# Performance work log

Hardware: AMD Instinct MI355X
Metric: run time of the kernel (lower is better)

## Reference

```python
import jax, jax.numpy as jnp
import numpy as np

B, C_HID, H, W = 2, 30, 1024, 1024
PS, PAD = 16, 4            # patch_size, patch_padding
MID, OUT = 80, 1
POST = 8                   # post_conv_layers
H_ERR, W_ERR = H // PS, W // PS
K_PER_B = int(H_ERR * W_ERR * 0.125)   # sampling top-k per batch = 512
P = B * K_PER_B
C_IN = C_HID + 1           # conv0 input channels = 31
KWIN = PS + 2 * PAD        # 24 = patch window incl. padding
N_PRE = PAD - 1            # conv1..conv3 (conv0 separate)
EPS = 1e-5


def _bn_params(key, c):
    k1, k2, k3, k4 = jax.random.split(key, 4)
    g = 1.0 + 0.1 * jax.random.normal(k1, (c,), jnp.float32)
    b = 0.1 * jax.random.normal(k2, (c,), jnp.float32)
    m = 0.1 * jax.random.normal(k3, (c,), jnp.float32)
    v = jax.random.uniform(k4, (c,), jnp.float32, 0.5, 1.5)
    return jnp.stack([g, b, m, v])  # (4, c)


def setup_inputs() -> dict:
    key = jax.random.key(0)
    ks = jax.random.split(key, 12)
    cw = lambda k, co, ci: 0.05 * jax.random.normal(k, (co, ci, 3, 3), jnp.float32)
    return {
        "pha": jax.random.normal(ks[0], (B, 1, H, W), jnp.float32),
        "err": jax.random.uniform(ks[1], (B, 1, H_ERR, W_ERR), jnp.float32),
        "hid": jax.random.normal(ks[2], (B, C_HID, H, W), jnp.float32),
        "w0": cw(ks[3], MID, C_IN),
        "bn0": _bn_params(ks[4], MID),
        "w_pre": 0.05 * jax.random.normal(ks[5], (N_PRE, MID, MID, 3, 3), jnp.float32),
        "bn_pre": jnp.stack([_bn_params(k, MID) for k in jax.random.split(ks[6], N_PRE)]),
        "w_post": 0.05 * jax.random.normal(ks[7], (POST - 1, MID, MID, 3, 3), jnp.float32),
        "bn_post": jnp.stack([_bn_params(k, MID) for k in jax.random.split(ks[8], POST - 1)]),
        "w_last": cw(ks[9], OUT, MID),
    }


def _conv(x, w, padding):
    return jax.lax.conv_general_dilated(x, w, (1, 1), padding,
        dimension_numbers=("NCHW", "OIHW", "NCHW"))


def _bn(x, p):  # eval-mode BatchNorm, p = (4, C)
    g, b, m, v = p
    inv = g * jax.lax.rsqrt(v + EPS)
    return x * inv[None, :, None, None] + (b - m * inv)[None, :, None, None]


def reference(pha, err, hid, w0, bn0, w_pre, bn_pre, w_post, bn_post, w_last):
    # --- select_refinement_regions (mode='sampling') ---
    err_flat = err.reshape(B, -1)                                   # (B, H_ERR*W_ERR)
    _, top_idx = jax.lax.top_k(err_flat, K_PER_B)                   # (B, K)
    ref = jnp.zeros_like(err_flat).at[jnp.arange(B)[:, None], top_idx].set(1.0)
    ref = ref * (err_flat > 0).astype(ref.dtype)                    # prevent_oversampling
    ref = ref.reshape(B, 1, H_ERR, W_ERR)
    # static-size nonzero: err>0 a.s. so exactly K per batch are selected
    b_idx = jnp.repeat(jnp.arange(B), K_PER_B)                      # (P,)
    flat = top_idx.reshape(-1)
    i_idx = flat // W_ERR
    j_idx = flat % W_ERR
    # --- crop_patch (unfold) on detached cat([hid, pha]) ---
    x = jax.lax.stop_gradient(jnp.concatenate([hid, pha], axis=1))  # (B, 31, H, W)
    xp = jnp.pad(x, ((0, 0), (0, 0), (PAD, PAD), (PAD, PAD)))
    rows = i_idx[:, None] * PS + jnp.arange(KWIN)[None, :]          # (P, 24)
    cols = j_idx[:, None] * PS + jnp.arange(KWIN)[None, :]
    patches = xp[b_idx[:, None, None], :, rows[:, :, None], cols[:, None, :]]  # (P,24,24,31)
    y = patches.transpose(0, 3, 1, 2)                               # (P, 31, 24, 24)
    # --- pre convs: valid 3x3, each shrinks by 2 (24 -> 16) ---
    y = jax.nn.relu(_bn(_conv(y, w0, "VALID"), bn0))
    for l in range(N_PRE):
        y = jax.nn.relu(_bn(_conv(y, w_pre[l], "VALID"), bn_pre[l]))
    # --- post convs: residual same-padded, last maps to out_channel ---
    for l in range(POST - 1):
        y = y + jax.nn.relu(_bn(_conv(y, w_post[l], "SAME"), bn_post[l]))
    y = _conv(y, w_last, "SAME")                                    # (P, 1, 16, 16)
    # --- replace_patch (scatter_nd) ---
    pha6 = pha.reshape(B, 1, H_ERR, PS, W_ERR, PS).transpose(0, 2, 4, 1, 3, 5)
    pha6 = pha6.at[b_idx, i_idx, j_idx].set(y)
    pha_out = pha6.transpose(0, 3, 1, 4, 2, 5).reshape(B, 1, H, W)
    return pha_out, ref
```

## Files before the change

kernel.cpp:

```cpp
#include <hip/hip_runtime.h>
#include <hip/hip_bf16.h>
#include <stdint.h>

typedef __hip_bfloat16 bf16;
typedef __attribute__((ext_vector_type(8))) short short8;
typedef __attribute__((ext_vector_type(4))) float f32x4;

__device__ __forceinline__ bf16 f2b(float x) { return __float2bfloat16(x); }

#define NW 8

#define A0_OFF 0
#define X_OFF  77440
#define A1_OFF 77440
#define A2_OFF 0
#define Z_OFF  57024
#define BB_OFF 114048
#define BS_OFF 147840
#define YF_OFF 0
#define SMEM_SZ 158080

__device__ __forceinline__ void gload_lds16(const void* g, char* l) {
    __builtin_amdgcn_global_load_lds(
        (const __attribute__((address_space(1))) unsigned int*)g,
        (__attribute__((address_space(3))) unsigned int*)l, 16, 0, 0);
}

__global__ __launch_bounds__(1024) void topk_kernel(const float* __restrict__ err,
                                                    float* __restrict__ ref_out,
                                                    int* __restrict__ sel)
{
    __shared__ uint64_t keys[4096];
    const int b = blockIdx.x >> 4, slice = blockIdx.x & 15;
    const float* e = err + b * 4096;
    for (int t = threadIdx.x; t < 4096; t += 1024) {
        uint32_t u = __float_as_uint(e[t]);
        u ^= (u >> 31) ? 0xFFFFFFFFu : 0x80000000u;
        keys[t] = ((uint64_t)u << 32) | (uint32_t)(4095 - t);
    }
    __syncthreads();
    const int cand = slice * 256 + (threadIdx.x >> 2);
    const int part = threadIdx.x & 3;
    const uint64_t mykey = keys[cand];
    int r = 0;
#pragma unroll 8
    for (int j = part * 1024; j < part * 1024 + 1024; ++j)
        r += (keys[j] > mykey) ? 1 : 0;
    r += __shfl_xor(r, 1);
    r += __shfl_xor(r, 2);
    if (part == 0) {
        bool s = (r < 512);
        if (s) sel[b * 512 + r] = cand;
        ref_out[b * 4096 + cand] = (s && e[cand] > 0.f) ? 1.f : 0.f;
    }
}

__global__ void wt_kernel(const float* __restrict__ w0, const float* __restrict__ wpre,
                          const float* __restrict__ wpost, const float* __restrict__ w_last,
                          const float* __restrict__ bn0, const float* __restrict__ bn_pre,
                          const float* __restrict__ bn_post,
                          bf16* __restrict__ Wf, float* __restrict__ wlastT,
                          float* __restrict__ bnprep)
{
    int t = blockIdx.x * blockDim.x + threadIdx.x;
    if (t < 714240) {
        int l, tap, kb, rem;
        if (t < 23040) { l = 0; tap = t / 2560; kb = 0; rem = t % 2560; }
        else {
            int t2 = t - 23040;
            l = 1 + t2 / 69120;
            int r0 = t2 % 69120;
            tap = r0 / 7680;
            int r1 = r0 % 7680;
            kb = r1 / 2560; rem = r1 % 2560;
        }
        int n = rem / 512, r2 = rem % 512, lane = r2 / 8, i = r2 % 8;
        int co = n * 16 + (lane & 15);
        int k  = kb * 32 + (lane >> 4) * 8 + i;
        float v = 0.f;
        if (l == 0)      { if (k < 31) v = w0[(co * 31 + k) * 9 + tap]; }
        else if (l <= 3) { if (k < 80) v = wpre[(((l - 1) * 80 + co) * 80 + k) * 9 + tap]; }
        else             { if (k < 80) v = wpost[(((l - 4) * 80 + co) * 80 + k) * 9 + tap]; }
        Wf[t] = f2b(v);
    } else if (t < 714960) {
        int i = t - 714240; int tap = i / 80, ci = i % 80;
        wlastT[tap * 80 + ci] = w_last[ci * 9 + tap];
    } else if (t < 715840) {
        int i = t - 714960; int l = i / 80, co = i % 80;
        const float* src = (l == 0) ? bn0 : (l <= 3 ? bn_pre + (l - 1) * 320
                                                    : bn_post + (l - 4) * 320);
        float g = src[co], bb = src[80 + co], m = src[160 + co], vv = src[240 + co];
        float inv = g * rsqrtf(vv + 1e-5f);
        bnprep[i * 2]     = inv;
        bnprep[i * 2 + 1] = bb - m * inv;
    }
}

__global__ void copy_kernel(const uint4* __restrict__ src, uint4* __restrict__ dst, int n)
{
    int t = blockIdx.x * blockDim.x + threadIdx.x;
    if (t < n) dst[t] = src[t];
}

template <int NIN, int NOUT, int KB, int PMAX, int MODE, int ISTR, int OSTR,
          int BIG, int STOREZ>
__device__ __forceinline__ void conv_mfma(char* sm, int inBase, int outBase,
                                          const char* __restrict__ Wl,
                                          const float* __restrict__ bnl,
                                          f32x4 (&Yreg)[2][5])
{
    const int tid = threadIdx.x;
    const int wv = tid >> 6, lane = tid & 63;
    const int r = lane & 15, kg = lane >> 4;
    constexpr int NPIX  = NOUT * NOUT;
    constexpr int NMT   = (NPIX + 15) / 16;
    constexpr int NSTEP = BIG ? 9 : 9 * KB;
    constexpr int SLOT  = BIG ? 16384 : 5120;
    constexpr int BOFF  = BIG ? BB_OFF : BS_OFF;
    constexpr int WSTEP = BIG ? 15360 : 5120;

    int aA[PMAX][2];
    bool act[PMAX][2];
#pragma unroll
    for (int pp = 0; pp < PMAX; ++pp)
#pragma unroll
        for (int mm = 0; mm < 2; ++mm) {
            int mt = (wv + pp * NW) * 2 + mm;
            int pix = mt * 16 + r;
            act[pp][mm] = (mt < NMT);
            int cp = pix < NPIX ? pix : NPIX - 1;
            aA[pp][mm] = inBase + ((cp / NOUT) * NIN + cp % NOUT) * ISTR + kg * 16;
        }
    const int vB = BOFF + lane * 16;

    float invb[5], betb[5];
#pragma unroll
    for (int n = 0; n < 5; ++n) {
        float2 v = ((const float2*)bnl)[n * 16 + r];
        invb[n] = v.x; betb[n] = v.y;
    }

    f32x4 zz = {0.f, 0.f, 0.f, 0.f};
    f32x4 acc[PMAX][2][5];
#pragma unroll
    for (int pp = 0; pp < PMAX; ++pp)
#pragma unroll
        for (int mm = 0; mm < 2; ++mm)
#pragma unroll
            for (int n = 0; n < 5; ++n) acc[pp][mm][n] = zz;

    auto stage = [&](int step, int slot) {
        const char* src = Wl + step * WSTEP;
        char* dst = sm + BOFF + slot * SLOT;
        if (BIG) {
            gload_lds16(src + tid * 16, dst + tid * 16);
            gload_lds16(src + 8192 + tid * 16, dst + 8192 + tid * 16);
        } else if (tid < 320) {
            gload_lds16(src + tid * 16, dst + tid * 16);
        }
    };

    auto inner = [&](int dtap, int kb, int slotBase) {
        short8 bf[5];
#pragma unroll
        for (int n = 0; n < 5; ++n)
            bf[n] = *(const short8*)(sm + slotBase + n * 1024 + lane * 16);
#pragma unroll
        for (int pp = 0; pp < PMAX; ++pp)
#pragma unroll
            for (int mm = 0; mm < 2; ++mm) {
                if (!act[pp][mm]) continue;
                short8 af = *(const short8*)(sm + aA[pp][mm] + dtap * ISTR + kb * 64);
#pragma unroll
                for (int n = 0; n < 5; ++n)
                    acc[pp][mm][n] = __builtin_amdgcn_mfma_f32_16x16x32_bf16(
                        af, bf[n], acc[pp][mm][n], 0, 0, 0);
            }
    };

    stage(0, 0);
    __syncthreads();

#pragma unroll
    for (int s = 0; s < NSTEP; ++s) {
        if (s + 1 < NSTEP) stage(s + 1, (s + 1) & 1);
        const int tap = BIG ? s : s / KB;
        const int dtap = (tap / 3) * NIN + (tap % 3);
        const int sb = BOFF + (s & 1) * SLOT;
        if (BIG) {
#pragma unroll
            for (int kb = 0; kb < 3; ++kb) inner(dtap, kb, sb + kb * 5120);
        } else {
            inner(dtap, s % KB, sb);
        }
        __syncthreads();
    }

#pragma unroll
    for (int pp = 0; pp < PMAX; ++pp)
#pragma unroll
        for (int mm = 0; mm < 2; ++mm) {
            int mt = (wv + pp * NW) * 2 + mm;
            if (mt < NMT) {
#pragma unroll
                for (int n = 0; n < 5; ++n) {
                    int co = n * 16 + r;
#pragma unroll
                    for (int j = 0; j < 4; ++j) {
                        int pix = mt * 16 + kg * 4 + j;
                        if (pix < NPIX) {
                            float o = fmaxf(acc[pp][mm][n][j] * invb[n] + betb[n], 0.f);
                            if (MODE == 0) {
                                *(bf16*)(sm + outBase + pix * OSTR + co * 2) = f2b(o);
                            } else if (MODE == 1) {
                                Yreg[mm][n][j] = o;
                                int rowb = ((pix >> 4) + 1) * (18 * 176) + ((pix & 15) + 1) * 176;
                                *(bf16*)(sm + outBase + rowb + co * 2) = f2b(o);
                            } else {
                                float nv = Yreg[mm][n][j] + o;
                                Yreg[mm][n][j] = nv;
                                if (STOREZ) {
                                    int rowb = ((pix >> 4) + 1) * (18 * 176) + ((pix & 15) + 1) * 176;
                                    *(bf16*)(sm + outBase + rowb + co * 2) = f2b(nv);
                                }
                            }
                        }
                    }
                }
            }
        }
}

__global__ __launch_bounds__(512, 2) void refine_kernel(
    const int* __restrict__ sel,
    const float* __restrict__ hid, const float* __restrict__ pha,
    const char* __restrict__ Wf, const float* __restrict__ wlastT,
    const float* __restrict__ bnprep, float* __restrict__ out)
{
    __shared__ __align__(16) char sm[SMEM_SZ];
    const int tid = threadIdx.x;
    const int p = blockIdx.x;
    const int e = sel[p];
    const int b = p >> 9;
    const int pi = e >> 6, pj = e & 63;

    {
        uint4 z4 = {0u, 0u, 0u, 0u};
        uint4* z = (uint4*)sm;
        for (int t = tid; t < SMEM_SZ / 16; t += 512) z[t] = z4;
    }
    __syncthreads();

    const int r0 = pi * 16 - 4, c0 = pj * 16 - 4;
    for (int t = tid; t < 32 * 576; t += 512) {
        int c = t / 576, pix = t - c * 576;
        int gr = r0 + pix / 24, gc = c0 + pix % 24;
        float v = 0.f;
        if (c < 31 && (unsigned)gr < 1024u && (unsigned)gc < 1024u)
            v = (c < 30) ? hid[((b * 30 + c) * 1024 + gr) * 1024 + gc]
                         : pha[(b * 1024 + gr) * 1024 + gc];
        *(bf16*)(sm + X_OFF + pix * 80 + c * 2) = f2b(v);
    }

    f32x4 Yreg[2][5];

    conv_mfma<24,22,1,2,0, 80,160,0,1>(sm, X_OFF,  A0_OFF, Wf,                    bnprep,       Yreg);
    conv_mfma<22,20,3,2,0,160,176,0,1>(sm, A0_OFF, A1_OFF, Wf + 46080,            bnprep + 160, Yreg);
    conv_mfma<20,18,3,2,0,176,176,0,1>(sm, A1_OFF, A2_OFF, Wf + 46080 + 138240,   bnprep + 320, Yreg);
    conv_mfma<18,16,3,1,1,176,176,1,1>(sm, A2_OFF, Z_OFF,  Wf + 46080 + 2*138240, bnprep + 480, Yreg);

    for (int t = tid; t < 68 * 44; t += 512) {
        int idx = t / 44, w = t - idx * 44;
        int row;
        if (idx < 18) row = idx;
        else if (idx < 36) row = 306 + (idx - 18);
        else { int k = idx - 36; row = (1 + (k >> 1)) * 18 + ((k & 1) ? 17 : 0); }
        *(uint32_t*)(sm + Z_OFF + row * 176 + w * 4) = 0u;
    }

#pragma unroll 1
    for (int l = 0; l < 6; ++l)
        conv_mfma<18,16,3,1,2,176,176,1,1>(sm, Z_OFF, Z_OFF,
                                           Wf + 46080 + (3 + l) * 138240,
                                           bnprep + 640 + l * 160, Yreg);
    conv_mfma<18,16,3,1,2,176,176,1,0>(sm, Z_OFF, Z_OFF,
                                       Wf + 46080 + 9 * 138240, bnprep + 1600, Yreg);

    {
        const int wv = tid >> 6, lane = tid & 63;
        const int r = lane & 15, kg = lane >> 4;
#pragma unroll
        for (int mm = 0; mm < 2; ++mm) {
            int mt = 2 * wv + mm;
#pragma unroll
            for (int n = 0; n < 5; ++n) {
                int co = n * 16 + r;
#pragma unroll
                for (int j = 0; j < 4; ++j) {
                    int pix = mt * 16 + kg * 4 + j;
                    *(float*)(sm + YF_OFF + pix * 336 + co * 4) = Yreg[mm][n][j];
                }
            }
        }
    }
    __syncthreads();

    {
        int pix = tid >> 1, half = tid & 1;
        int y = pix >> 4, x = pix & 15;
        float accv = 0.f;
        const float* Yb = (const float*)(sm + YF_OFF);
#pragma unroll
        for (int tap = 0; tap < 9; ++tap) {
            int iy = y + tap / 3 - 1, ix = x + tap % 3 - 1;
            if ((unsigned)iy >= 16u || (unsigned)ix >= 16u) continue;
            const float* yp = Yb + (iy * 16 + ix) * 84;
            const float* wp = wlastT + tap * 80;
            for (int c = half * 40; c < half * 40 + 40; c += 4) {
                float4 a  = *(const float4*)(yp + c);
                float4 w4 = *(const float4*)(wp + c);
                accv += a.x * w4.x + a.y * w4.y + a.z * w4.z + a.w * w4.w;
            }
        }
        accv += __shfl_xor(accv, 1);
        if (half == 0)
            out[b * 1048576 + (pi * 16 + y) * 1024 + pj * 16 + x] = accv;
    }
}

extern "C" void kernel_launch(void* const* d_in, const int* in_sizes, int n_in,
                              void* d_out, int out_size, void* d_ws, size_t ws_size,
                              hipStream_t stream)
{
    (void)in_sizes; (void)n_in; (void)out_size; (void)ws_size;
    const float* pha     = (const float*)d_in[0];
    const float* err     = (const float*)d_in[1];
    const float* hid     = (const float*)d_in[2];
    const float* w0      = (const float*)d_in[3];
    const float* bn0     = (const float*)d_in[4];
    const float* w_pre   = (const float*)d_in[5];
    const float* bn_pre  = (const float*)d_in[6];
    const float* w_post  = (const float*)d_in[7];
    const float* bn_post = (const float*)d_in[8];
    const float* w_last  = (const float*)d_in[9];
    float* out = (float*)d_out;

    char* ws = (char*)d_ws;
    bf16*  Wf     = (bf16*)ws;
    float* wlastT = (float*)(ws + 1429504);
    float* bnprep = (float*)(ws + 1432384);
    int*   sel    = (int*)(ws + 1441792);

    hipLaunchKernelGGL(wt_kernel, dim3(2797), dim3(256), 0, stream,
                       w0, w_pre, w_post, w_last, bn0, bn_pre, bn_post,
                       Wf, wlastT, bnprep);
    hipLaunchKernelGGL(topk_kernel, dim3(32), dim3(1024), 0, stream,
                       err, out + 2097152, sel);
    hipLaunchKernelGGL(copy_kernel, dim3(2048), dim3(256), 0, stream,
                       (const uint4*)pha, (uint4*)out, 524288);
    hipLaunchKernelGGL(refine_kernel, dim3(1024), dim3(512), 0, stream,
                       sel, hid, pha, (const char*)Wf, wlastT, bnprep, out);
}
```

Baseline: 510.5 us.

## Retile 16x16 post convs as 2D wave grid with DPP-shifted A-fragment reuse

Replaces the generic conv template for the last pre conv and the residual post convs with specialised kernels. These use a 4x2 wave grid (4 row tiles by 3 output-channel tiles, with channels padded to 96). In the post layers each wave loads 6 rows of A fragments once per K block and builds the dx-shifted operands with DPP lane shifts instead of re-reading LDS. Weights are relaid out per kb/tap in larger staged chunks. This cuts LDS reads per MFMA but adds padded-channel MFMAs (96 vs 80) and more barriers per layer.

```diff
diff --git a/kernel.cpp b/kernel.cpp
--- a/kernel.cpp
+++ b/kernel.cpp
@@ -11,19 +11,37 @@
 #define NW 8
 
 #define A0_OFF 0
-#define X_OFF  77440
-#define A1_OFF 77440
+#define X_OFF  81312
+#define A1_OFF 81312
 #define A2_OFF 0
 #define Z_OFF  57024
-#define BB_OFF 114048
-#define BS_OFF 147840
+#define B3_OFF 114048
+#define BS_OFF 151712
+#define BP_OFF 0
 #define YF_OFF 0
-#define SMEM_SZ 158080
+#define SMEM_SZ 161952
 
 __device__ __forceinline__ void gload_lds16(const void* g, char* l) {
     __builtin_amdgcn_global_load_lds(
         (const __attribute__((address_space(1))) unsigned int*)g,
         (__attribute__((address_space(3))) unsigned int*)l, 16, 0, 0);
+}
+
+__device__ __forceinline__ short8 dpp_sr1(short8 v) {
+    union { short8 s; int i[4]; } a, o;
+    a.s = v;
+#pragma unroll
+    for (int q = 0; q < 4; ++q)
+        o.i[q] = __builtin_amdgcn_mov_dpp(a.i[q], 0x111, 0xf, 0xf, true);
+    return o.s;
+}
+__device__ __forceinline__ short8 dpp_sl1(short8 v) {
+    union { short8 s; int i[4]; } a, o;
+    a.s = v;
+#pragma unroll
+    for (int q = 0; q < 4; ++q)
+        o.i[q] = __builtin_amdgcn_mov_dpp(a.i[q], 0x101, 0xf, 0xf, true);
+    return o.s;
 }
 
 __global__ __launch_bounds__(1024) void topk_kernel(const float* __restrict__ err,
@@ -63,36 +81,54 @@
                           float* __restrict__ bnprep)
 {
     int t = blockIdx.x * blockDim.x + threadIdx.x;
-    if (t < 714240) {
-        int l, tap, kb, rem;
-        if (t < 23040) { l = 0; tap = t / 2560; kb = 0; rem = t % 2560; }
-        else {
+    if (t < 824832) {
+        int co, k, tap;
+        float v = 0.f;
+        if (t < 23040) {
+            tap = t / 2560; int rem = t % 2560;
+            int n = rem / 512, r2 = rem % 512, lane = r2 / 8, i = r2 % 8;
+            co = n * 16 + (lane & 15); k = (lane >> 4) * 8 + i;
+            if (k < 31) v = w0[(co * 31 + k) * 9 + tap];
+        } else if (t < 161280) {
             int t2 = t - 23040;
-            l = 1 + t2 / 69120;
+            int l = t2 / 69120;
             int r0 = t2 % 69120;
-            tap = r0 / 7680;
-            int r1 = r0 % 7680;
-            kb = r1 / 2560; rem = r1 % 2560;
-        }
-        int n = rem / 512, r2 = rem % 512, lane = r2 / 8, i = r2 % 8;
-        int co = n * 16 + (lane & 15);
-        int k  = kb * 32 + (lane >> 4) * 8 + i;
-        float v = 0.f;
-        if (l == 0)      { if (k < 31) v = w0[(co * 31 + k) * 9 + tap]; }
-        else if (l <= 3) { if (k < 80) v = wpre[(((l - 1) * 80 + co) * 80 + k) * 9 + tap]; }
-        else             { if (k < 80) v = wpost[(((l - 4) * 80 + co) * 80 + k) * 9 + tap]; }
+            tap = r0 / 7680; int r1 = r0 % 7680;
+            int kb = r1 / 2560, rem = r1 % 2560;
+            int n = rem / 512, r2 = rem % 512, lane = r2 / 8, i = r2 % 8;
+            co = n * 16 + (lane & 15); k = kb * 32 + (lane >> 4) * 8 + i;
+            if (k < 80) v = wpre[((l * 80 + co) * 80 + k) * 9 + tap];
+        } else if (t < 244224) {
+            int t3 = t - 161280;
+            tap = t3 / 9216; int r0 = t3 % 9216;
+            int kb = r0 / 3072, rem = r0 % 3072;
+            int n = rem / 512, r2 = rem % 512, lane = r2 / 8, i = r2 % 8;
+            co = n * 16 + (lane & 15); k = kb * 32 + (lane >> 4) * 8 + i;
+            if (co < 80 && k < 80) v = wpre[((2 * 80 + co) * 80 + k) * 9 + tap];
+        } else {
+            int t4 = t - 244224;
+            int l = t4 / 82944; int r0 = t4 % 82944;
+            int kb = r0 / 27648; int r1 = r0 % 27648;
+            tap = r1 / 3072; int rem = r1 % 3072;
+            int n = rem / 512, r2 = rem % 512, lane = r2 / 8, i = r2 % 8;
+            co = n * 16 + (lane & 15); k = kb * 32 + (lane >> 4) * 8 + i;
+            if (co < 80 && k < 80) v = wpost[((l * 80 + co) * 80 + k) * 9 + tap];
+        }
         Wf[t] = f2b(v);
-    } else if (t < 714960) {
-        int i = t - 714240; int tap = i / 80, ci = i % 80;
+    } else if (t < 825552) {
+        int i = t - 824832; int tap = i / 80, ci = i % 80;
         wlastT[tap * 80 + ci] = w_last[ci * 9 + tap];
-    } else if (t < 715840) {
-        int i = t - 714960; int l = i / 80, co = i % 80;
-        const float* src = (l == 0) ? bn0 : (l <= 3 ? bn_pre + (l - 1) * 320
-                                                    : bn_post + (l - 4) * 320);
-        float g = src[co], bb = src[80 + co], m = src[160 + co], vv = src[240 + co];
-        float inv = g * rsqrtf(vv + 1e-5f);
-        bnprep[i * 2]     = inv;
-        bnprep[i * 2 + 1] = bb - m * inv;
+    } else if (t < 826608) {
+        int i = t - 825552; int l = i / 96, co = i % 96;
+        float inv = 0.f, beta = 0.f;
+        if (co < 80) {
+            const float* src = (l == 0) ? bn0 : (l <= 3 ? bn_pre + (l - 1) * 320
+                                                        : bn_post + (l - 4) * 320);
+            float g = src[co], bb = src[80 + co], m = src[160 + co], vv = src[240 + co];
+            inv = g * rsqrtf(vv + 1e-5f);
+            beta = bb - m * inv;
+        }
+        bnprep[i * 2] = inv; bnprep[i * 2 + 1] = beta;
     }
 }
 
@@ -102,27 +138,22 @@
     if (t < n) dst[t] = src[t];
 }
 
-template <int NIN, int NOUT, int KB, int PMAX, int MODE, int ISTR, int OSTR,
-          int BIG, int STOREZ>
-__device__ __forceinline__ void conv_mfma(char* sm, int inBase, int outBase,
-                                          const char* __restrict__ Wl,
-                                          const float* __restrict__ bnl,
-                                          f32x4 (&Yreg)[2][5])
+template <int NIN, int NOUT, int KB, int ISTR, int OSTR>
+__device__ __forceinline__ void conv_small(char* sm, int inBase, int outBase,
+                                           const char* __restrict__ Wl,
+                                           const float* __restrict__ bnl)
 {
     const int tid = threadIdx.x;
     const int wv = tid >> 6, lane = tid & 63;
     const int r = lane & 15, kg = lane >> 4;
-    constexpr int NPIX  = NOUT * NOUT;
-    constexpr int NMT   = (NPIX + 15) / 16;
-    constexpr int NSTEP = BIG ? 9 : 9 * KB;
-    constexpr int SLOT  = BIG ? 16384 : 5120;
-    constexpr int BOFF  = BIG ? BB_OFF : BS_OFF;
-    constexpr int WSTEP = BIG ? 15360 : 5120;
-
-    int aA[PMAX][2];
-    bool act[PMAX][2];
-#pragma unroll
-    for (int pp = 0; pp < PMAX; ++pp)
+    constexpr int NPIX = NOUT * NOUT;
+    constexpr int NMT = (NPIX + 15) / 16;
+    constexpr int NSTEP = 9 * KB;
+
+    int aA[2][2];
+    bool act[2][2];
+#pragma unroll
+    for (int pp = 0; pp < 2; ++pp)
 #pragma unroll
         for (int mm = 0; mm < 2; ++mm) {
             int mt = (wv + pp * NW) * 2 + mm;
@@ -131,7 +162,6 @@
             int cp = pix < NPIX ? pix : NPIX - 1;
             aA[pp][mm] = inBase + ((cp / NOUT) * NIN + cp % NOUT) * ISTR + kg * 16;
         }
-    const int vB = BOFF + lane * 16;
 
     float invb[5], betb[5];
 #pragma unroll
@@ -141,32 +171,35 @@
     }
 
     f32x4 zz = {0.f, 0.f, 0.f, 0.f};
-    f32x4 acc[PMAX][2][5];
-#pragma unroll
-    for (int pp = 0; pp < PMAX; ++pp)
+    f32x4 acc[2][2][5];
+#pragma unroll
+    for (int pp = 0; pp < 2; ++pp)
 #pragma unroll
         for (int mm = 0; mm < 2; ++mm)
 #pragma unroll
             for (int n = 0; n < 5; ++n) acc[pp][mm][n] = zz;
 
-    auto stage = [&](int step, int slot) {
-        const char* src = Wl + step * WSTEP;
-        char* dst = sm + BOFF + slot * SLOT;
-        if (BIG) {
-            gload_lds16(src + tid * 16, dst + tid * 16);
-            gload_lds16(src + 8192 + tid * 16, dst + 8192 + tid * 16);
-        } else if (tid < 320) {
-            gload_lds16(src + tid * 16, dst + tid * 16);
-        }
+    auto stage = [&](int step) {
+        if (tid < 320)
+            gload_lds16(Wl + step * 5120 + tid * 16,
+                        sm + BS_OFF + (step & 1) * 5120 + tid * 16);
     };
 
-    auto inner = [&](int dtap, int kb, int slotBase) {
+    stage(0);
+    __syncthreads();
+
+#pragma unroll
+    for (int s = 0; s < NSTEP; ++s) {
+        if (s + 1 < NSTEP) stage(s + 1);
+        const int tap = s / KB, kb = s % KB;
+        const int dtap = (tap / 3) * NIN + (tap % 3);
+        const int sb = BS_OFF + (s & 1) * 5120;
         short8 bf[5];
 #pragma unroll
         for (int n = 0; n < 5; ++n)
-            bf[n] = *(const short8*)(sm + slotBase + n * 1024 + lane * 16);
-#pragma unroll
-        for (int pp = 0; pp < PMAX; ++pp)
+            bf[n] = *(const short8*)(sm + sb + n * 1024 + lane * 16);
+#pragma unroll
+        for (int pp = 0; pp < 2; ++pp)
 #pragma unroll
             for (int mm = 0; mm < 2; ++mm) {
                 if (!act[pp][mm]) continue;
@@ -176,28 +209,11 @@
                     acc[pp][mm][n] = __builtin_amdgcn_mfma_f32_16x16x32_bf16(
                         af, bf[n], acc[pp][mm][n], 0, 0, 0);
             }
-    };
-
-    stage(0, 0);
-    __syncthreads();
-
-#pragma unroll
-    for (int s = 0; s < NSTEP; ++s) {
-        if (s + 1 < NSTEP) stage(s + 1, (s + 1) & 1);
-        const int tap = BIG ? s : s / KB;
-        const int dtap = (tap / 3) * NIN + (tap % 3);
-        const int sb = BOFF + (s & 1) * SLOT;
-        if (BIG) {
-#pragma unroll
-            for (int kb = 0; kb < 3; ++kb) inner(dtap, kb, sb + kb * 5120);
-        } else {
-            inner(dtap, s % KB, sb);
-        }
         __syncthreads();
     }
 
 #pragma unroll
-    for (int pp = 0; pp < PMAX; ++pp)
+    for (int pp = 0; pp < 2; ++pp)
 #pragma unroll
         for (int mm = 0; mm < 2; ++mm) {
             int mt = (wv + pp * NW) * 2 + mm;
@@ -210,23 +226,201 @@
                         int pix = mt * 16 + kg * 4 + j;
                         if (pix < NPIX) {
                             float o = fmaxf(acc[pp][mm][n][j] * invb[n] + betb[n], 0.f);
-                            if (MODE == 0) {
-                                *(bf16*)(sm + outBase + pix * OSTR + co * 2) = f2b(o);
-                            } else if (MODE == 1) {
-                                Yreg[mm][n][j] = o;
-                                int rowb = ((pix >> 4) + 1) * (18 * 176) + ((pix & 15) + 1) * 176;
-                                *(bf16*)(sm + outBase + rowb + co * 2) = f2b(o);
-                            } else {
-                                float nv = Yreg[mm][n][j] + o;
-                                Yreg[mm][n][j] = nv;
-                                if (STOREZ) {
-                                    int rowb = ((pix >> 4) + 1) * (18 * 176) + ((pix & 15) + 1) * 176;
-                                    *(bf16*)(sm + outBase + rowb + co * 2) = f2b(nv);
-                                }
-                            }
+                            *(bf16*)(sm + outBase + pix * OSTR + co * 2) = f2b(o);
                         }
                     }
                 }
+            }
+        }
+}
+
+__device__ __forceinline__ void pre3_conv(char* sm, const char* __restrict__ Wl,
+                                          const float* __restrict__ bnl,
+                                          f32x4 (&Yreg)[4][3])
+{
+    const int tid = threadIdx.x;
+    const int wv = tid >> 6, lane = tid & 63;
+    const int r = lane & 15, kg = lane >> 4;
+    const int wm = wv & 3, wn = wv >> 2;
+
+    float invb[3], betb[3];
+#pragma unroll
+    for (int n = 0; n < 3; ++n) {
+        float2 v = ((const float2*)bnl)[(3 * wn + n) * 16 + r];
+        invb[n] = v.x; betb[n] = v.y;
+    }
+
+    f32x4 zz = {0.f, 0.f, 0.f, 0.f};
+    f32x4 acc[4][3];
+#pragma unroll
+    for (int mm = 0; mm < 4; ++mm)
+#pragma unroll
+        for (int n = 0; n < 3; ++n) acc[mm][n] = zz;
+
+    auto stage = [&](int tap) {
+        const char* src = Wl + tap * 18432;
+        char* dst = sm + B3_OFF + (tap & 1) * 18432;
+#pragma unroll
+        for (int it = 0; it < 3; ++it) {
+            int off = it * 8192 + tid * 16;
+            if (off < 18432) gload_lds16(src + off, dst + off);
+        }
+    };
+
+    stage(0);
+    __syncthreads();
+
+#pragma unroll
+    for (int tap = 0; tap < 9; ++tap) {
+        if (tap + 1 < 9) stage(tap + 1);
+        const int dy = tap / 3, dx = tap % 3;
+        const int slotB = B3_OFF + (tap & 1) * 18432;
+#pragma unroll
+        for (int kb = 0; kb < 3; ++kb) {
+            short8 bf[3];
+#pragma unroll
+            for (int n = 0; n < 3; ++n)
+                bf[n] = *(const short8*)(sm + slotB + (kb * 6 + 3 * wn + n) * 1024 + lane * 16);
+#pragma unroll
+            for (int mm = 0; mm < 4; ++mm) {
+                short8 af = *(const short8*)(sm + A2_OFF +
+                    ((4 * wm + mm + dy) * 18 + r + dx) * 176 + kb * 64 + kg * 16);
+#pragma unroll
+                for (int n = 0; n < 3; ++n)
+                    acc[mm][n] = __builtin_amdgcn_mfma_f32_16x16x32_bf16(
+                        af, bf[n], acc[mm][n], 0, 0, 0);
+            }
+        }
+        __syncthreads();
+    }
+
+#pragma unroll
+    for (int mm = 0; mm < 4; ++mm)
+#pragma unroll
+        for (int n = 0; n < 3; ++n) {
+            int co = (3 * wn + n) * 16 + r;
+            bool keep = (3 * wn + n) < 5;
+            int y = 4 * wm + mm;
+#pragma unroll
+            for (int j = 0; j < 4; ++j) {
+                int x = kg * 4 + j;
+                float o = fmaxf(acc[mm][n][j] * invb[n] + betb[n], 0.f);
+                Yreg[mm][n][j] = o;
+                if (keep)
+                    *(bf16*)(sm + Z_OFF + ((y + 1) * 18 + x + 1) * 176 + co * 2) = f2b(o);
+            }
+        }
+}
+
+template <int LAST>
+__device__ __forceinline__ void post_layer(char* sm, const char* __restrict__ Wl,
+                                           const float* __restrict__ bnl,
+                                           f32x4 (&Yreg)[4][3])
+{
+    const int tid = threadIdx.x;
+    const int wv = tid >> 6, lane = tid & 63;
+    const int r = lane & 15, kg = lane >> 4;
+    const int wm = wv & 3, wn = wv >> 2;
+
+    float invb[3], betb[3];
+#pragma unroll
+    for (int n = 0; n < 3; ++n) {
+        float2 v = ((const float2*)bnl)[(3 * wn + n) * 16 + r];
+        invb[n] = v.x; betb[n] = v.y;
+    }
+
+    f32x4 zz = {0.f, 0.f, 0.f, 0.f};
+    f32x4 acc[4][3];
+#pragma unroll
+    for (int mm = 0; mm < 4; ++mm)
+#pragma unroll
+        for (int n = 0; n < 3; ++n) acc[mm][n] = zz;
+
+    auto fill0 = [&](int kb) {
+#pragma unroll
+        for (int it = 0; it < 4; ++it) {
+            int off = it * 8192 + tid * 16;
+            if (off < 30720) gload_lds16(Wl + kb * 55296 + off, sm + BP_OFF + off);
+        }
+    };
+    auto fill1 = [&](int kb) {
+#pragma unroll
+        for (int it = 0; it < 3; ++it) {
+            int off = it * 8192 + tid * 16;
+            gload_lds16(Wl + kb * 55296 + 30720 + off, sm + BP_OFF + 30720 + off);
+        }
+    };
+
+    const int cBase = Z_OFF + (4 * wm * 18 + 1 + r) * 176 + kg * 16;
+
+    fill0(0);
+    __syncthreads();
+
+#pragma unroll
+    for (int kb = 0; kb < 3; ++kb) {
+        short8 C[6];
+#pragma unroll
+        for (int u = 0; u < 6; ++u)
+            C[u] = *(const short8*)(sm + cBase + u * 3168 + kb * 64);
+
+        fill1(kb);
+#pragma unroll
+        for (int tap = 0; tap < 5; ++tap) {
+            const int dy = tap / 3, dx = tap % 3;
+            short8 bf[3];
+#pragma unroll
+            for (int n = 0; n < 3; ++n)
+                bf[n] = *(const short8*)(sm + BP_OFF + tap * 6144 + (3 * wn + n) * 1024 + lane * 16);
+#pragma unroll
+            for (int mm = 0; mm < 4; ++mm) {
+                short8 af = C[mm + dy];
+                if (dx == 0) af = dpp_sr1(af);
+                else if (dx == 2) af = dpp_sl1(af);
+#pragma unroll
+                for (int n = 0; n < 3; ++n)
+                    acc[mm][n] = __builtin_amdgcn_mfma_f32_16x16x32_bf16(
+                        af, bf[n], acc[mm][n], 0, 0, 0);
+            }
+        }
+        __syncthreads();
+
+        if (kb < 2) fill0(kb + 1);
+#pragma unroll
+        for (int tap = 5; tap < 9; ++tap) {
+            const int dy = tap / 3, dx = tap % 3;
+            short8 bf[3];
+#pragma unroll
+            for (int n = 0; n < 3; ++n)
+                bf[n] = *(const short8*)(sm + BP_OFF + 30720 + (tap - 5) * 6144 + (3 * wn + n) * 1024 + lane * 16);
+#pragma unroll
+            for (int mm = 0; mm < 4; ++mm) {
+                short8 af = C[mm + dy];
+                if (dx == 0) af = dpp_sr1(af);
+                else if (dx == 2) af = dpp_sl1(af);
+#pragma unroll
+                for (int n = 0; n < 3; ++n)
+                    acc[mm][n] = __builtin_amdgcn_mfma_f32_16x16x32_bf16(
+                        af, bf[n], acc[mm][n], 0, 0, 0);
+            }
+        }
+        __syncthreads();
+    }
+
+#pragma unroll
+    for (int mm = 0; mm < 4; ++mm)
+#pragma unroll
+        for (int n = 0; n < 3; ++n) {
+            int co = (3 * wn + n) * 16 + r;
+            bool keep = (3 * wn + n) < 5;
+            int y = 4 * wm + mm;
+#pragma unroll
+            for (int j = 0; j < 4; ++j) {
+                int x = kg * 4 + j;
+                float o = fmaxf(acc[mm][n][j] * invb[n] + betb[n], 0.f);
+                float nv = Yreg[mm][n][j] + o;
+                Yreg[mm][n][j] = nv;
+                if (!LAST && keep)
+                    *(bf16*)(sm + Z_OFF + ((y + 1) * 18 + x + 1) * 176 + co * 2) = f2b(nv);
             }
         }
 }
@@ -262,46 +456,44 @@
         *(bf16*)(sm + X_OFF + pix * 80 + c * 2) = f2b(v);
     }
 
-    f32x4 Yreg[2][5];
-
-    conv_mfma<24,22,1,2,0, 80,160,0,1>(sm, X_OFF,  A0_OFF, Wf,                    bnprep,       Yreg);
-    conv_mfma<22,20,3,2,0,160,176,0,1>(sm, A0_OFF, A1_OFF, Wf + 46080,            bnprep + 160, Yreg);
-    conv_mfma<20,18,3,2,0,176,176,0,1>(sm, A1_OFF, A2_OFF, Wf + 46080 + 138240,   bnprep + 320, Yreg);
-    conv_mfma<18,16,3,1,1,176,176,1,1>(sm, A2_OFF, Z_OFF,  Wf + 46080 + 2*138240, bnprep + 480, Yreg);
-
-    for (int t = tid; t < 68 * 44; t += 512) {
-        int idx = t / 44, w = t - idx * 44;
-        int row;
-        if (idx < 18) row = idx;
-        else if (idx < 36) row = 306 + (idx - 18);
-        else { int k = idx - 36; row = (1 + (k >> 1)) * 18 + ((k & 1) ? 17 : 0); }
-        *(uint32_t*)(sm + Z_OFF + row * 176 + w * 4) = 0u;
-    }
+    conv_small<24, 22, 1,  80, 168>(sm, X_OFF,  A0_OFF, Wf,          bnprep);
+    conv_small<22, 20, 3, 168, 176>(sm, A0_OFF, A1_OFF, Wf + 46080,  bnprep + 192);
+    conv_small<20, 18, 3, 176, 176>(sm, A1_OFF, A2_OFF, Wf + 184320, bnprep + 384);
+
+    for (int t = tid; t < 68 * 11; t += 512) {
+        int cell = t / 11, part = t % 11;
+        int i, j;
+        if (cell < 18)      { i = 0;  j = cell; }
+        else if (cell < 36) { i = 17; j = cell - 18; }
+        else { int k = cell - 36; i = 1 + (k >> 1); j = (k & 1) ? 17 : 0; }
+        *(uint4*)(sm + Z_OFF + (i * 18 + j) * 176 + part * 16) = (uint4){0u, 0u, 0u, 0u};
+    }
+
+    f32x4 Yreg[4][3];
+    pre3_conv(sm, Wf + 322560, bnprep + 576, Yreg);
 
 #pragma unroll 1
     for (int l = 0; l < 6; ++l)
-        conv_mfma<18,16,3,1,2,176,176,1,1>(sm, Z_OFF, Z_OFF,
-                                           Wf + 46080 + (3 + l) * 138240,
-                                           bnprep + 640 + l * 160, Yreg);
-    conv_mfma<18,16,3,1,2,176,176,1,0>(sm, Z_OFF, Z_OFF,
-                                       Wf + 46080 + 9 * 138240, bnprep + 1600, Yreg);
+        post_layer<0>(sm, Wf + 488448 + l * 165888, bnprep + 768 + l * 192, Yreg);
+    post_layer<1>(sm, Wf + 488448 + 6 * 165888, bnprep + 768 + 6 * 192, Yreg);
 
     {
         const int wv = tid >> 6, lane = tid & 63;
         const int r = lane & 15, kg = lane >> 4;
-#pragma unroll
-        for (int mm = 0; mm < 2; ++mm) {
-            int mt = 2 * wv + mm;
-#pragma unroll
-            for (int n = 0; n < 5; ++n) {
-                int co = n * 16 + r;
-#pragma unroll
-                for (int j = 0; j < 4; ++j) {
-                    int pix = mt * 16 + kg * 4 + j;
-                    *(float*)(sm + YF_OFF + pix * 336 + co * 4) = Yreg[mm][n][j];
+        const int wm = wv & 3, wn = wv >> 2;
+#pragma unroll
+        for (int mm = 0; mm < 4; ++mm)
+#pragma unroll
+            for (int n = 0; n < 3; ++n) {
+                int co = (3 * wn + n) * 16 + r;
+                if ((3 * wn + n) < 5) {
+#pragma unroll
+                    for (int j = 0; j < 4; ++j) {
+                        int pix = (4 * wm + mm) * 16 + kg * 4 + j;
+                        *(float*)(sm + YF_OFF + pix * 336 + co * 4) = Yreg[mm][n][j];
+                    }
                 }
             }
-        }
     }
     __syncthreads();
 
@@ -347,11 +539,11 @@
 
     char* ws = (char*)d_ws;
     bf16*  Wf     = (bf16*)ws;
-    float* wlastT = (float*)(ws + 1429504);
-    float* bnprep = (float*)(ws + 1432384);
-    int*   sel    = (int*)(ws + 1441792);
-
-    hipLaunchKernelGGL(wt_kernel, dim3(2797), dim3(256), 0, stream,
+    float* wlastT = (float*)(ws + 1649664);
+    float* bnprep = (float*)(ws + 1652544);
+    int*   sel    = (int*)(ws + 1661056);
+
+    hipLaunchKernelGGL(wt_kernel, dim3(3230), dim3(256), 0, stream,
                        w0, w_pre, w_post, w_last, bn0, bn_pre, bn_post,
                        Wf, wlastT, bnprep);
     hipLaunchKernelGGL(topk_kernel, dim3(32), dim3(1024), 0, stream,
```

After: 572.1 us. +12.1%, slower.

## Fold BN scale into weights, triple-buffer weight staging, retile big convs onto four waves

Applied to the files above, without the earlier changes.

The weight prep kernel now multiplies each conv weight by its BatchNorm scale, so accumulators start at the BN bias and the epilogue is only a ReLU. Weight staging into LDS moves from double to triple buffering with a prefetch distance of two, using explicit vmcnt/lgkmcnt waits plus a raw s_barrier. This is meant to hide global-to-LDS latency and cut the number of full syncs. The 16x16 residual convs are split out into a separate routine in which only four waves compute, each over four row m-tiles, so each B fragment load is reused across more MFMAs. The trade-off is that half the waves sit idle during those layers. Border zeroing now uses 16-byte stores, and LDS usage grows to 163200 bytes.

```diff
diff --git a/kernel.cpp b/kernel.cpp
--- a/kernel.cpp
+++ b/kernel.cpp
@@ -18,7 +18,7 @@
 #define BB_OFF 114048
 #define BS_OFF 147840
 #define YF_OFF 0
-#define SMEM_SZ 158080
+#define SMEM_SZ 163200
 
 __device__ __forceinline__ void gload_lds16(const void* g, char* l) {
     __builtin_amdgcn_global_load_lds(
@@ -60,7 +60,7 @@
                           const float* __restrict__ bn0, const float* __restrict__ bn_pre,
                           const float* __restrict__ bn_post,
                           bf16* __restrict__ Wf, float* __restrict__ wlastT,
-                          float* __restrict__ bnprep)
+                          float* __restrict__ bnbeta)
 {
     int t = blockIdx.x * blockDim.x + threadIdx.x;
     if (t < 714240) {
@@ -81,7 +81,10 @@
         if (l == 0)      { if (k < 31) v = w0[(co * 31 + k) * 9 + tap]; }
         else if (l <= 3) { if (k < 80) v = wpre[(((l - 1) * 80 + co) * 80 + k) * 9 + tap]; }
         else             { if (k < 80) v = wpost[(((l - 4) * 80 + co) * 80 + k) * 9 + tap]; }
-        Wf[t] = f2b(v);
+        const float* src = (l == 0) ? bn0 : (l <= 3 ? bn_pre + (l - 1) * 320
+                                                    : bn_post + (l - 4) * 320);
+        float inv = src[co] * rsqrtf(src[240 + co] + 1e-5f);
+        Wf[t] = f2b(v * inv);
     } else if (t < 714960) {
         int i = t - 714240; int tap = i / 80, ci = i % 80;
         wlastT[tap * 80 + ci] = w_last[ci * 9 + tap];
@@ -89,10 +92,8 @@
         int i = t - 714960; int l = i / 80, co = i % 80;
         const float* src = (l == 0) ? bn0 : (l <= 3 ? bn_pre + (l - 1) * 320
                                                     : bn_post + (l - 4) * 320);
-        float g = src[co], bb = src[80 + co], m = src[160 + co], vv = src[240 + co];
-        float inv = g * rsqrtf(vv + 1e-5f);
-        bnprep[i * 2]     = inv;
-        bnprep[i * 2 + 1] = bb - m * inv;
+        float inv = src[co] * rsqrtf(src[240 + co] + 1e-5f);
+        bnbeta[i] = src[80 + co] - src[160 + co] * inv;
     }
 }
 
@@ -102,27 +103,22 @@
     if (t < n) dst[t] = src[t];
 }
 
-template <int NIN, int NOUT, int KB, int PMAX, int MODE, int ISTR, int OSTR,
-          int BIG, int STOREZ>
-__device__ __forceinline__ void conv_mfma(char* sm, int inBase, int outBase,
-                                          const char* __restrict__ Wl,
-                                          const float* __restrict__ bnl,
-                                          f32x4 (&Yreg)[2][5])
+template <int NIN, int NOUT, int KB, int ISTR, int OSTR>
+__device__ __forceinline__ void conv_small(char* sm, int inBase, int outBase,
+                                           const char* __restrict__ Wl,
+                                           const float* __restrict__ bnl)
 {
     const int tid = threadIdx.x;
     const int wv = tid >> 6, lane = tid & 63;
     const int r = lane & 15, kg = lane >> 4;
-    constexpr int NPIX  = NOUT * NOUT;
-    constexpr int NMT   = (NPIX + 15) / 16;
-    constexpr int NSTEP = BIG ? 9 : 9 * KB;
-    constexpr int SLOT  = BIG ? 16384 : 5120;
-    constexpr int BOFF  = BIG ? BB_OFF : BS_OFF;
-    constexpr int WSTEP = BIG ? 15360 : 5120;
-
-    int aA[PMAX][2];
-    bool act[PMAX][2];
-#pragma unroll
-    for (int pp = 0; pp < PMAX; ++pp)
+    constexpr int NPIX = NOUT * NOUT;
+    constexpr int NMT = (NPIX + 15) / 16;
+    constexpr int NSTEP = 9 * KB;
+
+    int aA[2][2];
+    bool act[2][2];
+#pragma unroll
+    for (int pp = 0; pp < 2; ++pp)
 #pragma unroll
         for (int mm = 0; mm < 2; ++mm) {
             int mt = (wv + pp * NW) * 2 + mm;
@@ -131,42 +127,45 @@
             int cp = pix < NPIX ? pix : NPIX - 1;
             aA[pp][mm] = inBase + ((cp / NOUT) * NIN + cp % NOUT) * ISTR + kg * 16;
         }
-    const int vB = BOFF + lane * 16;
-
-    float invb[5], betb[5];
-#pragma unroll
-    for (int n = 0; n < 5; ++n) {
-        float2 v = ((const float2*)bnl)[n * 16 + r];
-        invb[n] = v.x; betb[n] = v.y;
-    }
-
-    f32x4 zz = {0.f, 0.f, 0.f, 0.f};
-    f32x4 acc[PMAX][2][5];
-#pragma unroll
-    for (int pp = 0; pp < PMAX; ++pp)
+
+    float betb[5];
+#pragma unroll
+    for (int n = 0; n < 5; ++n) betb[n] = bnl[n * 16 + r];
+
+    f32x4 acc[2][2][5];
+#pragma unroll
+    for (int pp = 0; pp < 2; ++pp)
 #pragma unroll
         for (int mm = 0; mm < 2; ++mm)
 #pragma unroll
-            for (int n = 0; n < 5; ++n) acc[pp][mm][n] = zz;
-
-    auto stage = [&](int step, int slot) {
-        const char* src = Wl + step * WSTEP;
-        char* dst = sm + BOFF + slot * SLOT;
-        if (BIG) {
-            gload_lds16(src + tid * 16, dst + tid * 16);
-            gload_lds16(src + 8192 + tid * 16, dst + 8192 + tid * 16);
-        } else if (tid < 320) {
-            gload_lds16(src + tid * 16, dst + tid * 16);
-        }
+            for (int n = 0; n < 5; ++n) {
+                f32x4 bi = {betb[n], betb[n], betb[n], betb[n]};
+                acc[pp][mm][n] = bi;
+            }
+
+    auto stage = [&](int step) {
+        if (tid < 320)
+            gload_lds16(Wl + step * 5120 + tid * 16,
+                        sm + BS_OFF + (step % 3) * 5120 + tid * 16);
     };
 
-    auto inner = [&](int dtap, int kb, int slotBase) {
+    asm volatile("s_waitcnt vmcnt(0)" ::: "memory");
+    stage(0); stage(1);
+    asm volatile("s_waitcnt vmcnt(1) lgkmcnt(0)" ::: "memory");
+    __builtin_amdgcn_s_barrier();
+
+#pragma unroll
+    for (int s = 0; s < NSTEP; ++s) {
+        if (s + 2 < NSTEP) stage(s + 2);
+        const int tap = s / KB, kb = s % KB;
+        const int dtap = (tap / 3) * NIN + (tap % 3);
+        const int sb = BS_OFF + (s % 3) * 5120;
         short8 bf[5];
 #pragma unroll
         for (int n = 0; n < 5; ++n)
-            bf[n] = *(const short8*)(sm + slotBase + n * 1024 + lane * 16);
-#pragma unroll
-        for (int pp = 0; pp < PMAX; ++pp)
+            bf[n] = *(const short8*)(sm + sb + n * 1024 + lane * 16);
+#pragma unroll
+        for (int pp = 0; pp < 2; ++pp)
 #pragma unroll
             for (int mm = 0; mm < 2; ++mm) {
                 if (!act[pp][mm]) continue;
@@ -176,28 +175,15 @@
                     acc[pp][mm][n] = __builtin_amdgcn_mfma_f32_16x16x32_bf16(
                         af, bf[n], acc[pp][mm][n], 0, 0, 0);
             }
-    };
-
-    stage(0, 0);
-    __syncthreads();
-
-#pragma unroll
-    for (int s = 0; s < NSTEP; ++s) {
-        if (s + 1 < NSTEP) stage(s + 1, (s + 1) & 1);
-        const int tap = BIG ? s : s / KB;
-        const int dtap = (tap / 3) * NIN + (tap % 3);
-        const int sb = BOFF + (s & 1) * SLOT;
-        if (BIG) {
-#pragma unroll
-            for (int kb = 0; kb < 3; ++kb) inner(dtap, kb, sb + kb * 5120);
-        } else {
-            inner(dtap, s % KB, sb);
-        }
-        __syncthreads();
-    }
-
-#pragma unroll
-    for (int pp = 0; pp < PMAX; ++pp)
+        if (s + 2 < NSTEP)
+            asm volatile("s_waitcnt vmcnt(1) lgkmcnt(0)" ::: "memory");
+        else
+            asm volatile("s_waitcnt vmcnt(0) lgkmcnt(0)" ::: "memory");
+        __builtin_amdgcn_s_barrier();
+    }
+
+#pragma unroll
+    for (int pp = 0; pp < 2; ++pp)
 #pragma unroll
         for (int mm = 0; mm < 2; ++mm) {
             int mt = (wv + pp * NW) * 2 + mm;
@@ -209,33 +195,116 @@
                     for (int j = 0; j < 4; ++j) {
                         int pix = mt * 16 + kg * 4 + j;
                         if (pix < NPIX) {
-                            float o = fmaxf(acc[pp][mm][n][j] * invb[n] + betb[n], 0.f);
-                            if (MODE == 0) {
-                                *(bf16*)(sm + outBase + pix * OSTR + co * 2) = f2b(o);
-                            } else if (MODE == 1) {
-                                Yreg[mm][n][j] = o;
-                                int rowb = ((pix >> 4) + 1) * (18 * 176) + ((pix & 15) + 1) * 176;
-                                *(bf16*)(sm + outBase + rowb + co * 2) = f2b(o);
-                            } else {
-                                float nv = Yreg[mm][n][j] + o;
-                                Yreg[mm][n][j] = nv;
-                                if (STOREZ) {
-                                    int rowb = ((pix >> 4) + 1) * (18 * 176) + ((pix & 15) + 1) * 176;
-                                    *(bf16*)(sm + outBase + rowb + co * 2) = f2b(nv);
-                                }
-                            }
+                            float o = fmaxf(acc[pp][mm][n][j], 0.f);
+                            *(bf16*)(sm + outBase + pix * OSTR + co * 2) = f2b(o);
                         }
                     }
                 }
             }
         }
+}
+
+template <int MODE, int STOREZ>
+__device__ __forceinline__ void conv_big(char* sm, int inBase,
+                                         const char* __restrict__ Wl,
+                                         const float* __restrict__ bnl,
+                                         f32x4 (&Yreg)[4][5])
+{
+    const int tid = threadIdx.x;
+    const int wv = tid >> 6, lane = tid & 63;
+    const int r = lane & 15, kg = lane >> 4;
+    const bool cw = (wv < 4);
+
+    float betb[5];
+#pragma unroll
+    for (int n = 0; n < 5; ++n) betb[n] = bnl[n * 16 + r];
+
+    f32x4 acc[4][5];
+#pragma unroll
+    for (int mm = 0; mm < 4; ++mm)
+#pragma unroll
+        for (int n = 0; n < 5; ++n) {
+            f32x4 bi = {betb[n], betb[n], betb[n], betb[n]};
+            acc[mm][n] = bi;
+        }
+
+    int aBase[4];
+#pragma unroll
+    for (int mm = 0; mm < 4; ++mm)
+        aBase[mm] = inBase + (((wv & 3) * 4 + mm) * 18 + r) * 176 + kg * 16;
+
+    auto stage = [&](int step) {
+        const char* src = Wl + step * 15360;
+        char* dst = sm + BB_OFF + (step % 3) * 16384;
+        gload_lds16(src + tid * 16, dst + tid * 16);
+        gload_lds16(src + 8192 + tid * 16, dst + 8192 + tid * 16);
+    };
+
+    asm volatile("s_waitcnt vmcnt(0)" ::: "memory");
+    stage(0); stage(1);
+    asm volatile("s_waitcnt vmcnt(2) lgkmcnt(0)" ::: "memory");
+    __builtin_amdgcn_s_barrier();
+
+#pragma unroll
+    for (int s = 0; s < 9; ++s) {
+        if (s + 2 < 9) stage(s + 2);
+        if (cw) {
+            const int dt = ((s / 3) * 18 + (s % 3)) * 176;
+            const int sb = BB_OFF + (s % 3) * 16384;
+#pragma unroll
+            for (int kb = 0; kb < 3; ++kb) {
+                short8 bf[5];
+#pragma unroll
+                for (int n = 0; n < 5; ++n)
+                    bf[n] = *(const short8*)(sm + sb + kb * 5120 + n * 1024 + lane * 16);
+#pragma unroll
+                for (int mm = 0; mm < 4; ++mm) {
+                    short8 af = *(const short8*)(sm + aBase[mm] + dt + kb * 64);
+#pragma unroll
+                    for (int n = 0; n < 5; ++n)
+                        acc[mm][n] = __builtin_amdgcn_mfma_f32_16x16x32_bf16(
+                            af, bf[n], acc[mm][n], 0, 0, 0);
+                }
+            }
+        }
+        if (s + 2 < 9)
+            asm volatile("s_waitcnt vmcnt(2) lgkmcnt(0)" ::: "memory");
+        else
+            asm volatile("s_waitcnt vmcnt(0) lgkmcnt(0)" ::: "memory");
+        __builtin_amdgcn_s_barrier();
+    }
+
+    if (cw) {
+#pragma unroll
+        for (int mm = 0; mm < 4; ++mm) {
+            int y = wv * 4 + mm;
+#pragma unroll
+            for (int n = 0; n < 5; ++n) {
+                int co = n * 16 + r;
+#pragma unroll
+                for (int j = 0; j < 4; ++j) {
+                    int x = kg * 4 + j;
+                    float o = fmaxf(acc[mm][n][j], 0.f);
+                    if (MODE == 1) {
+                        Yreg[mm][n][j] = o;
+                        *(bf16*)(sm + Z_OFF + ((y + 1) * 18 + x + 1) * 176 + co * 2) = f2b(o);
+                    } else {
+                        float nv = Yreg[mm][n][j] + o;
+                        Yreg[mm][n][j] = nv;
+                        if (STOREZ)
+                            *(bf16*)(sm + Z_OFF + ((y + 1) * 18 + x + 1) * 176 + co * 2) = f2b(nv);
+                    }
+                }
+            }
+        }
+    }
 }
 
 __global__ __launch_bounds__(512, 2) void refine_kernel(
     const int* __restrict__ sel,
     const float* __restrict__ hid, const float* __restrict__ pha,
     const char* __restrict__ Wf, const float* __restrict__ wlastT,
-    const float* __restrict__ bnprep, float* __restrict__ out)
+    const float* __restrict__ bnbeta, float* __restrict__ out)
 {
     __shared__ __align__(16) char sm[SMEM_SZ];
     const int tid = threadIdx.x;
@@ -262,45 +331,41 @@
         *(bf16*)(sm + X_OFF + pix * 80 + c * 2) = f2b(v);
     }
 
-    f32x4 Yreg[2][5];
-
-    conv_mfma<24,22,1,2,0, 80,160,0,1>(sm, X_OFF,  A0_OFF, Wf,                    bnprep,       Yreg);
-    conv_mfma<22,20,3,2,0,160,176,0,1>(sm, A0_OFF, A1_OFF, Wf + 46080,            bnprep + 160, Yreg);
-    conv_mfma<20,18,3,2,0,176,176,0,1>(sm, A1_OFF, A2_OFF, Wf + 46080 + 138240,   bnprep + 320, Yreg);
-    conv_mfma<18,16,3,1,1,176,176,1,1>(sm, A2_OFF, Z_OFF,  Wf + 46080 + 2*138240, bnprep + 480, Yreg);
-
-    for (int t = tid; t < 68 * 44; t += 512) {
-        int idx = t / 44, w = t - idx * 44;
-        int row;
-        if (idx < 18) row = idx;
-        else if (idx < 36) row = 306 + (idx - 18);
-        else { int k = idx - 36; row = (1 + (k >> 1)) * 18 + ((k & 1) ? 17 : 0); }
-        *(uint32_t*)(sm + Z_OFF + row * 176 + w * 4) = 0u;
-    }
-
+    conv_small<24, 22, 1,  80, 160>(sm, X_OFF,  A0_OFF, Wf,          bnbeta);
+    conv_small<22, 20, 3, 160, 176>(sm, A0_OFF, A1_OFF, Wf + 46080,  bnbeta + 80);
+    conv_small<20, 18, 3, 176, 176>(sm, A1_OFF, A2_OFF, Wf + 184320, bnbeta + 160);
+
+    for (int t = tid; t < 68 * 11; t += 512) {
+        int cell = t / 11, part = t % 11;
+        int i, j;
+        if (cell < 18)      { i = 0;  j = cell; }
+        else if (cell < 36) { i = 17; j = cell - 18; }
+        else { int k = cell - 36; i = 1 + (k >> 1); j = (k & 1) ? 17 : 0; }
+        *(uint4*)(sm + Z_OFF + (i * 18 + j) * 176 + part * 16) = (uint4){0u, 0u, 0u, 0u};
+    }
+
+    f32x4 Yreg[4][5];
+    conv_big<1, 1>(sm, A2_OFF, Wf + 322560, bnbeta + 240, Yreg);
 #pragma unroll 1
     for (int l = 0; l < 6; ++l)
-        conv_mfma<18,16,3,1,2,176,176,1,1>(sm, Z_OFF, Z_OFF,
-                                           Wf + 46080 + (3 + l) * 138240,
-                                           bnprep + 640 + l * 160, Yreg);
-    conv_mfma<18,16,3,1,2,176,176,1,0>(sm, Z_OFF, Z_OFF,
-                                       Wf + 46080 + 9 * 138240, bnprep + 1600, Yreg);
+        conv_big<2, 1>(sm, Z_OFF, Wf + 460800 + l * 138240, bnbeta + 320 + l * 80, Yreg);
+    conv_big<2, 0>(sm, Z_OFF, Wf + 460800 + 6 * 138240, bnbeta + 800, Yreg);
 
     {
         const int wv = tid >> 6, lane = tid & 63;
         const int r = lane & 15, kg = lane >> 4;
-#pragma unroll
-        for (int mm = 0; mm < 2; ++mm) {
-            int mt = 2 * wv + mm;
-#pragma unroll
-            for (int n = 0; n < 5; ++n) {
-                int co = n * 16 + r;
-#pragma unroll
-                for (int j = 0; j < 4; ++j) {
-                    int pix = mt * 16 + kg * 4 + j;
-                    *(float*)(sm + YF_OFF + pix * 336 + co * 4) = Yreg[mm][n][j];
+        if (wv < 4) {
+#pragma unroll
+            for (int mm = 0; mm < 4; ++mm)
+#pragma unroll
+                for (int n = 0; n < 5; ++n) {
+                    int co = n * 16 + r;
+#pragma unroll
+                    for (int j = 0; j < 4; ++j) {
+                        int pix = (wv * 4 + mm) * 16 + kg * 4 + j;
+                        *(float*)(sm + YF_OFF + pix * 336 + co * 4) = Yreg[mm][n][j];
+                    }
                 }
-            }
         }
     }
     __syncthreads();
@@ -348,16 +413,16 @@
     char* ws = (char*)d_ws;
     bf16*  Wf     = (bf16*)ws;
     float* wlastT = (float*)(ws + 1429504);
-    float* bnprep = (float*)(ws + 1432384);
+    float* bnbeta = (float*)(ws + 1432384);
     int*   sel    = (int*)(ws + 1441792);
 
     hipLaunchKernelGGL(wt_kernel, dim3(2797), dim3(256), 0, stream,
                        w0, w_pre, w_post, w_last, bn0, bn_pre, bn_post,
-                       Wf, wlastT, bnprep);
+                       Wf, wlastT, bnbeta);
     hipLaunchKernelGGL(topk_kernel, dim3(32), dim3(1024), 0, stream,
                        err, out + 2097152, sel);
     hipLaunchKernelGGL(copy_kernel, dim3(2048), dim3(256), 0, stream,
                        (const uint4*)pha, (uint4*)out, 524288);
     hipLaunchKernelGGL(refine_kernel, dim3(1024), dim3(512), 0, stream,
-                       sel, hid, pha, (const char*)Wf, wlastT, bnprep, out);
-}
+                       sel, hid, pha, (const char*)Wf, wlastT, bnbeta, out);
+}
```

Result: slower. 665.6 us (+30.4%).
